# Kernel tuning notes

Measured on AMD Instinct MI355X. Metric: run time of the kernel, lower is better.

The kernel has to match this reference:

```python
import jax
import jax.numpy as jnp
import numpy as np

TOKENS, D_IN, D_OUT = 8192, 4096, 4096
QMAX = 127.0


def setup_inputs() -> dict:
    key = jax.random.key(0)
    k_x, k_w, k_s, k_o, k_b = jax.random.split(key, 5)
    x = jax.random.normal(k_x, (TOKENS, D_IN), dtype=jnp.float32)
    # int8-valued weight stored as int32 for portability (values in [-127, 127])
    weight = jax.random.randint(k_w, (D_OUT, D_IN), -127, 128, dtype=jnp.int32)
    # realistic small per-channel dequant scales
    weight_scale = (jax.random.uniform(k_s, (D_OUT,), dtype=jnp.float32) + 0.5) * 0.01
    # module stores -weight_offset; keep small integer-ish zero points
    weight_offset = jnp.round(jax.random.normal(k_o, (D_OUT,), dtype=jnp.float32) * 4.0)
    bias = jax.random.normal(k_b, (D_OUT,), dtype=jnp.float32) * 0.1
    return {"x": x, "weight": weight, "weight_scale": weight_scale,
            "weight_offset": weight_offset, "bias": bias}


def reference(x, weight, weight_scale, weight_offset, bias):
    # --- dynamic per-token symmetric activation quantization ---
    act_scale = jnp.max(jnp.abs(x), axis=-1, keepdims=True) / QMAX   # [T, 1]
    x_q = jnp.clip(jnp.round(x / act_scale), -QMAX, QMAX)            # int-valued fp32 [T, D_in]

    # --- int8 GEMM with per-channel zero-point correction ---
    # stored weight_offset = -zero_point, so dequant weight = scale * (w_q + weight_offset)
    acc = x_q @ weight.astype(jnp.float32).T                          # [T, D_out]
    zp_corr = jnp.sum(x_q, axis=-1, keepdims=True) * weight_offset[None, :]
    acc = acc + zp_corr

    # --- dequant + bias epilogue ---
    y = acc * act_scale * weight_scale[None, :] + bias[None, :]
    return y
```

## Files before the change

### kernel.cpp

```cpp
#include <hip/hip_runtime.h>
#include <cstdint>
#include <cstddef>

#define TOKENS 8192
#define DIN    4096
#define DOUT   4096

typedef int int4v  __attribute__((ext_vector_type(4)));
typedef int int16v __attribute__((ext_vector_type(16)));

__global__ __launch_bounds__(256) void quant_rows(const float* __restrict__ x,
                                                  int* __restrict__ xq,
                                                  float* __restrict__ ascale,
                                                  int* __restrict__ rsum) {
  const int row = blockIdx.x;
  const int t = threadIdx.x;
  const float4* xr = (const float4*)(x + (size_t)row * DIN);
  float4 v[4];
#pragma unroll
  for (int i = 0; i < 4; ++i) v[i] = xr[i * 256 + t];

  float m = 0.f;
#pragma unroll
  for (int i = 0; i < 4; ++i) {
    m = fmaxf(m, fabsf(v[i].x)); m = fmaxf(m, fabsf(v[i].y));
    m = fmaxf(m, fabsf(v[i].z)); m = fmaxf(m, fabsf(v[i].w));
  }
#pragma unroll
  for (int off = 32; off; off >>= 1) m = fmaxf(m, __shfl_xor(m, off));

  __shared__ float wmax[4];
  __shared__ int   wsum[4];
  const int lane = t & 63, wid = t >> 6;
  if (lane == 0) wmax[wid] = m;
  __syncthreads();
  m = fmaxf(fmaxf(wmax[0], wmax[1]), fmaxf(wmax[2], wmax[3]));

  const float s = m * (1.0f / 127.0f);
  const float sdiv = (m > 0.f) ? s : 1.0f;

  int ssum = 0;
#pragma unroll
  for (int i = 0; i < 4; ++i) {
    float q;
    q = fminf(fmaxf(rintf(v[i].x / sdiv), -127.f), 127.f); const int b0 = (int)q;
    q = fminf(fmaxf(rintf(v[i].y / sdiv), -127.f), 127.f); const int b1 = (int)q;
    q = fminf(fmaxf(rintf(v[i].z / sdiv), -127.f), 127.f); const int b2 = (int)q;
    q = fminf(fmaxf(rintf(v[i].w / sdiv), -127.f), 127.f); const int b3 = (int)q;
    ssum += b0 + b1 + b2 + b3;
    xq[(size_t)row * 1024 + i * 256 + t] =
        (b0 & 255) | ((b1 & 255) << 8) | ((b2 & 255) << 16) | ((b3 & 255) << 24);
  }
#pragma unroll
  for (int off = 32; off; off >>= 1) ssum += __shfl_xor(ssum, off);
  if (lane == 0) wsum[wid] = ssum;
  __syncthreads();
  if (t == 0) {
    rsum[row]   = wsum[0] + wsum[1] + wsum[2] + wsum[3];
    ascale[row] = s;
  }
}

__global__ __launch_bounds__(256) void wconv(const int* __restrict__ w,
                                             int* __restrict__ w8) {
  const int idx = blockIdx.x * 256 + threadIdx.x;
  const int4 v = ((const int4*)w)[idx];
  w8[idx] = (v.x & 255) | ((v.y & 255) << 8) | ((v.z & 255) << 16) | ((v.w & 255) << 24);
}

__device__ __forceinline__ void gload_lds16(const char* g, char* l) {
  __builtin_amdgcn_global_load_lds(
      (const __attribute__((address_space(1))) void*)g,
      (__attribute__((address_space(3))) void*)l, 16, 0, 0);
}

#define MFMA8(AV, BV)                                                         \
  __builtin_amdgcn_s_setprio(1);                                              \
  _Pragma("unroll")                                                           \
  for (int mi = 0; mi < 4; ++mi)                                              \
    _Pragma("unroll")                                                         \
    for (int ni = 0; ni < 2; ++ni)                                            \
      acc[mi][ni] = __builtin_amdgcn_mfma_i32_32x32x32_i8(                    \
          AV[mi], BV[ni], acc[mi][ni], 0, 0, 0);                              \
  __builtin_amdgcn_s_setprio(0);

#define TILE_BODY(T_, STAGE_, VMN_, NEXT_)                                    \
  do {                                                                        \
    const char* Lb = lds + ((T_) & 3) * 32768;                                \
    char* Wb = lds + (((T_) + 3) & 3) * 32768;                                \
    if (STAGE_) {                                                             \
      const size_t ko = (size_t)((T_) + 3) * 64;                              \
      gload_lds16(gA0 + ko, Wb + ldst);                                       \
      gload_lds16(gA1 + ko, Wb + 8192 + ldst);                                \
      gload_lds16(gB0 + ko, Wb + 16384 + ldst);                               \
      gload_lds16(gB1 + ko, Wb + 24576 + ldst);                               \
    }                                                                         \
    _Pragma("unroll")                                                         \
    for (int mi = 0; mi < 4; ++mi)                                            \
      aB[mi] = *(const int4v*)(Lb + aoff1 + mi * 2048);                       \
    _Pragma("unroll")                                                         \
    for (int ni = 0; ni < 2; ++ni)                                            \
      bB[ni] = *(const int4v*)(Lb + boff1 + ni * 2048);                       \
    MFMA8(aA, bA)                                                             \
    if (NEXT_) {                                                              \
      const char* Ln = lds + (((T_) + 1) & 3) * 32768;                        \
      _Pragma("unroll")                                                       \
      for (int mi = 0; mi < 4; ++mi)                                          \
        aA[mi] = *(const int4v*)(Ln + aoff0 + mi * 2048);                     \
      _Pragma("unroll")                                                       \
      for (int ni = 0; ni < 2; ++ni)                                          \
        bA[ni] = *(const int4v*)(Ln + boff0 + ni * 2048);                     \
    }                                                                         \
    MFMA8(aB, bB)                                                             \
    if ((VMN_) >= 0) {                                                        \
      if ((VMN_) == 4)      asm volatile("s_waitcnt vmcnt(4)" ::: "memory");  \
      else if ((VMN_) == 0) asm volatile("s_waitcnt vmcnt(0)" ::: "memory");  \
      __builtin_amdgcn_s_barrier();                                           \
    }                                                                         \
  } while (0)

__global__ __launch_bounds__(512, 2) void gemm_i8(
    const char* __restrict__ xq, const char* __restrict__ w8,
    const float* __restrict__ ascale, const int* __restrict__ rsum,
    const float* __restrict__ wscale, const float* __restrict__ woff,
    const float* __restrict__ bias, float* __restrict__ y) {

  __shared__ __align__(16) char lds[131072];

  const int bid = blockIdx.x;
  const int tm = bid >> 4;
  const int tn = bid & 15;
  const int t = threadIdx.x;
  const int lane = t & 63, wid = t >> 6;
  const int wmI = wid >> 2;
  const int wnI = wid & 3;

  const int S = (t * 16) ^ (((t >> 3) & 3) << 4) ^ (((t >> 6) & 1) << 6);
  const int srow = S >> 6;
  const int scol = S & 63;

  const char* gA0 = xq + (size_t)(tm * 256 + srow) * DIN + scol;
  const char* gA1 = gA0 + (size_t)128 * DIN;
  const char* gB0 = w8 + (size_t)(tn * 256 + srow) * DIN + scol;
  const char* gB1 = gB0 + (size_t)128 * DIN;
  const int ldst = t * 16;

  const int mask  = (((lane >> 1) & 3) << 4) ^ (((lane >> 4) & 1) << 6);
  const int arow  = (lane & 31) * 64 + (lane >> 5) * 16;
  const int aoff0 = wmI * 8192 + ((arow +  0) ^ mask);
  const int aoff1 = wmI * 8192 + ((arow + 32) ^ mask);
  const int brow  = (wnI & 1) * 4096 + arow;
  const int boff0 = (2 + (wnI >> 1)) * 8192 + ((brow +  0) ^ mask);
  const int boff1 = (2 + (wnI >> 1)) * 8192 + ((brow + 32) ^ mask);

  int16v acc[4][2];
#pragma unroll
  for (int mi = 0; mi < 4; ++mi)
#pragma unroll
    for (int ni = 0; ni < 2; ++ni)
#pragma unroll
      for (int rg = 0; rg < 16; ++rg) acc[mi][ni][rg] = 0;

  int4v aA[4], bA[2], aB[4], bB[2];

#pragma unroll
  for (int p = 0; p < 3; ++p) {
    char* Wb = lds + p * 32768;
    gload_lds16(gA0 + p * 64, Wb + ldst);
    gload_lds16(gA1 + p * 64, Wb + 8192 + ldst);
    gload_lds16(gB0 + p * 64, Wb + 16384 + ldst);
    gload_lds16(gB1 + p * 64, Wb + 24576 + ldst);
  }
  asm volatile("s_waitcnt vmcnt(4)" ::: "memory");
  __builtin_amdgcn_s_barrier();
#pragma unroll
  for (int mi = 0; mi < 4; ++mi) aA[mi] = *(const int4v*)(lds + aoff0 + mi * 2048);
#pragma unroll
  for (int ni = 0; ni < 2; ++ni) bA[ni] = *(const int4v*)(lds + boff0 + ni * 2048);

  for (int T = 0; T < 61; ++T) TILE_BODY(T, 1, 4, 1);
  TILE_BODY(61, 0, 0, 1);
  TILE_BODY(62, 0, -1, 1);
  TILE_BODY(63, 0, -1, 0);

  const int rb0 = tm * 256 + wmI * 128 + 4 * (lane >> 5);
  const int cb0 = tn * 256 + wnI * 64 + (lane & 31);
  const float ws0 = wscale[cb0],      ws1 = wscale[cb0 + 32];
  const float wo0 = woff[cb0],        wo1 = woff[cb0 + 32];
  const float bi0 = bias[cb0],        bi1 = bias[cb0 + 32];
#pragma unroll
  for (int mi = 0; mi < 4; ++mi) {
#pragma unroll
    for (int rg = 0; rg < 16; ++rg) {
      const int r = rb0 + mi * 32 + (rg & 3) + 8 * (rg >> 2);
      const float as_ = ascale[r];
      const float rs_ = (float)rsum[r];
      y[(size_t)r * DOUT + cb0]      = ((float)acc[mi][0][rg] + rs_ * wo0) * (as_ * ws0) + bi0;
      y[(size_t)r * DOUT + cb0 + 32] = ((float)acc[mi][1][rg] + rs_ * wo1) * (as_ * ws1) + bi1;
    }
  }
}

extern "C" void kernel_launch(void* const* d_in, const int* in_sizes, int n_in,
                              void* d_out, int out_size, void* d_ws, size_t ws_size,
                              hipStream_t stream) {
  const float* x      = (const float*)d_in[0];
  const int*   w      = (const int*)  d_in[1];
  const float* wscale = (const float*)d_in[2];
  const float* woff   = (const float*)d_in[3];
  const float* bias   = (const float*)d_in[4];
  float* y = (float*)d_out;

  char* ws = (char*)d_ws;
  char*  xq     = ws;
  char*  w8     = ws + (size_t)TOKENS * DIN;
  float* ascale = (float*)(w8 + (size_t)DOUT * DIN);
  int*   rsum   = (int*)(ascale + TOKENS);

  hipLaunchKernelGGL(quant_rows, dim3(TOKENS), dim3(256), 0, stream,
                     x, (int*)xq, ascale, rsum);
  hipLaunchKernelGGL(wconv, dim3((DOUT * DIN / 4) / 256), dim3(256), 0, stream,
                     w, (int*)w8);
  hipLaunchKernelGGL(gemm_i8, dim3((TOKENS / 256) * (DOUT / 256)), dim3(512), 0, stream,
                     xq, w8, ascale, rsum, wscale, woff, bias, y);
}
```

Before: 201.6 us.

## Load B operand directly from global into registers, stage only A via LDS

The weight (B) tile is no longer staged through LDS. Each wave now loads its own B fragments straight from global memory into registers, double-buffered one k-step ahead, while A keeps the LDS pipeline with half the LDS footprint. This removes the LDS traffic and bank pressure for B and frees LDS capacity. In exchange, B rows are reloaded from global/L2 by every wave that shares them instead of being shared through LDS. The vmcnt wait counts are adjusted to match the new number of in-flight loads.

```diff
diff --git a/kernel.cpp b/kernel.cpp
--- a/kernel.cpp
+++ b/kernel.cpp
@@ -68,55 +68,52 @@
   w8[idx] = (v.x & 255) | ((v.y & 255) << 8) | ((v.z & 255) << 16) | ((v.w & 255) << 24);
 }
 
-__device__ __forceinline__ void gload_lds16(const char* g, char* l) {
-  __builtin_amdgcn_global_load_lds(
-      (const __attribute__((address_space(1))) void*)g,
-      (__attribute__((address_space(3))) void*)l, 16, 0, 0);
-}
-
-#define MFMA8(AV, BV)                                                         \
-  __builtin_amdgcn_s_setprio(1);                                              \
-  _Pragma("unroll")                                                           \
-  for (int mi = 0; mi < 4; ++mi)                                              \
-    _Pragma("unroll")                                                         \
-    for (int ni = 0; ni < 2; ++ni)                                            \
-      acc[mi][ni] = __builtin_amdgcn_mfma_i32_32x32x32_i8(                    \
-          AV[mi], BV[ni], acc[mi][ni], 0, 0, 0);                              \
-  __builtin_amdgcn_s_setprio(0);
-
-#define TILE_BODY(T_, STAGE_, VMN_, NEXT_)                                    \
+#define GLOAD(G_, L_) __builtin_amdgcn_global_load_lds(                       \
+      (const __attribute__((address_space(1))) void*)(G_),                    \
+      (__attribute__((address_space(3))) void*)(L_), 16, 0, 0)
+
+#define TILE_BODY(T_, BC_, BN_, STG_, LDB_, LDA_, VMN_)                       \
   do {                                                                        \
-    const char* Lb = lds + ((T_) & 3) * 32768;                                \
-    char* Wb = lds + (((T_) + 3) & 3) * 32768;                                \
-    if (STAGE_) {                                                             \
+    const int rbO = ((T_) & 3) * 16384;                                       \
+    if (STG_) {                                                               \
+      char* Wb = lds + (((T_) + 3) & 3) * 16384;                              \
       const size_t ko = (size_t)((T_) + 3) * 64;                              \
-      gload_lds16(gA0 + ko, Wb + ldst);                                       \
-      gload_lds16(gA1 + ko, Wb + 8192 + ldst);                                \
-      gload_lds16(gB0 + ko, Wb + 16384 + ldst);                               \
-      gload_lds16(gB1 + ko, Wb + 24576 + ldst);                               \
+      GLOAD(gA0 + ko, Wb + ldst);                                             \
+      GLOAD(gA1 + ko, Wb + 8192 + ldst);                                      \
+    }                                                                         \
+    if (LDB_) {                                                               \
+      const size_t kb = (size_t)((T_) + 1) * 64;                              \
+      BN_[0] = *(const int4v*)(gB00 + kb);                                    \
+      BN_[1] = *(const int4v*)(gB10 + kb);                                    \
+      BN_[2] = *(const int4v*)(gB01 + kb);                                    \
+      BN_[3] = *(const int4v*)(gB11 + kb);                                    \
     }                                                                         \
     _Pragma("unroll")                                                         \
     for (int mi = 0; mi < 4; ++mi)                                            \
-      aB[mi] = *(const int4v*)(Lb + aoff1 + mi * 2048);                       \
+      aB[mi] = *(const int4v*)(lds + rbO + aoff1 + mi * 2048);                \
+    __builtin_amdgcn_s_setprio(1);                                            \
     _Pragma("unroll")                                                         \
-    for (int ni = 0; ni < 2; ++ni)                                            \
-      bB[ni] = *(const int4v*)(Lb + boff1 + ni * 2048);                       \
-    MFMA8(aA, bA)                                                             \
-    if (NEXT_) {                                                              \
-      const char* Ln = lds + (((T_) + 1) & 3) * 32768;                        \
+    for (int mi = 0; mi < 4; ++mi) {                                          \
+      acc[mi][0] = __builtin_amdgcn_mfma_i32_32x32x32_i8(aA[mi], BC_[0], acc[mi][0], 0, 0, 0); \
+      acc[mi][1] = __builtin_amdgcn_mfma_i32_32x32x32_i8(aA[mi], BC_[1], acc[mi][1], 0, 0, 0); \
+    }                                                                         \
+    __builtin_amdgcn_s_setprio(0);                                            \
+    if (LDA_) {                                                               \
+      const int rnO = (((T_) + 1) & 3) * 16384;                               \
       _Pragma("unroll")                                                       \
       for (int mi = 0; mi < 4; ++mi)                                          \
-        aA[mi] = *(const int4v*)(Ln + aoff0 + mi * 2048);                     \
-      _Pragma("unroll")                                                       \
-      for (int ni = 0; ni < 2; ++ni)                                          \
-        bA[ni] = *(const int4v*)(Ln + boff0 + ni * 2048);                     \
-    }                                                                         \
-    MFMA8(aB, bB)                                                             \
-    if ((VMN_) >= 0) {                                                        \
-      if ((VMN_) == 4)      asm volatile("s_waitcnt vmcnt(4)" ::: "memory");  \
-      else if ((VMN_) == 0) asm volatile("s_waitcnt vmcnt(0)" ::: "memory");  \
-      __builtin_amdgcn_s_barrier();                                           \
-    }                                                                         \
+        aA[mi] = *(const int4v*)(lds + rnO + aoff0 + mi * 2048);              \
+    }                                                                         \
+    __builtin_amdgcn_s_setprio(1);                                            \
+    _Pragma("unroll")                                                         \
+    for (int mi = 0; mi < 4; ++mi) {                                          \
+      acc[mi][0] = __builtin_amdgcn_mfma_i32_32x32x32_i8(aB[mi], BC_[2], acc[mi][0], 0, 0, 0); \
+      acc[mi][1] = __builtin_amdgcn_mfma_i32_32x32x32_i8(aB[mi], BC_[3], acc[mi][1], 0, 0, 0); \
+    }                                                                         \
+    __builtin_amdgcn_s_setprio(0);                                            \
+    if ((VMN_) == 6)      asm volatile("s_waitcnt vmcnt(6)" ::: "memory");    \
+    else if ((VMN_) == 4) asm volatile("s_waitcnt vmcnt(4)" ::: "memory");    \
+    if ((VMN_) >= 0) __builtin_amdgcn_s_barrier();                            \
   } while (0)
 
 __global__ __launch_bounds__(512, 2) void gemm_i8(
@@ -125,7 +122,7 @@
     const float* __restrict__ wscale, const float* __restrict__ woff,
     const float* __restrict__ bias, float* __restrict__ y) {
 
-  __shared__ __align__(16) char lds[131072];
+  __shared__ __align__(16) char lds[65536];
 
   const int bid = blockIdx.x;
   const int tm = bid >> 4;
@@ -141,17 +138,19 @@
 
   const char* gA0 = xq + (size_t)(tm * 256 + srow) * DIN + scol;
   const char* gA1 = gA0 + (size_t)128 * DIN;
-  const char* gB0 = w8 + (size_t)(tn * 256 + srow) * DIN + scol;
-  const char* gB1 = gB0 + (size_t)128 * DIN;
   const int ldst = t * 16;
 
   const int mask  = (((lane >> 1) & 3) << 4) ^ (((lane >> 4) & 1) << 6);
   const int arow  = (lane & 31) * 64 + (lane >> 5) * 16;
   const int aoff0 = wmI * 8192 + ((arow +  0) ^ mask);
   const int aoff1 = wmI * 8192 + ((arow + 32) ^ mask);
-  const int brow  = (wnI & 1) * 4096 + arow;
-  const int boff0 = (2 + (wnI >> 1)) * 8192 + ((brow +  0) ^ mask);
-  const int boff1 = (2 + (wnI >> 1)) * 8192 + ((brow + 32) ^ mask);
+
+  const char* gBL = w8 + (size_t)(tn * 256 + wnI * 64 + (lane & 31)) * DIN
+                       + (lane >> 5) * 16;
+  const char* gB00 = gBL;
+  const char* gB10 = gBL + 32 * DIN;
+  const char* gB01 = gBL + 32;
+  const char* gB11 = gBL + 32 * DIN + 32;
 
   int16v acc[4][2];
 #pragma unroll
@@ -161,27 +160,32 @@
 #pragma unroll
       for (int rg = 0; rg < 16; ++rg) acc[mi][ni][rg] = 0;
 
-  int4v aA[4], bA[2], aB[4], bB[2];
-
+  int4v aA[4], aB[4], bC[4], bN[4];
+
+  bC[0] = *(const int4v*)gB00;
+  bC[1] = *(const int4v*)gB10;
+  bC[2] = *(const int4v*)gB01;
+  bC[3] = *(const int4v*)gB11;
 #pragma unroll
   for (int p = 0; p < 3; ++p) {
-    char* Wb = lds + p * 32768;
-    gload_lds16(gA0 + p * 64, Wb + ldst);
-    gload_lds16(gA1 + p * 64, Wb + 8192 + ldst);
-    gload_lds16(gB0 + p * 64, Wb + 16384 + ldst);
-    gload_lds16(gB1 + p * 64, Wb + 24576 + ldst);
-  }
-  asm volatile("s_waitcnt vmcnt(4)" ::: "memory");
+    char* Wb = lds + p * 16384;
+    GLOAD(gA0 + p * 64, Wb + ldst);
+    GLOAD(gA1 + p * 64, Wb + 8192 + ldst);
+  }
+  asm volatile("s_waitcnt vmcnt(2)" ::: "memory");
   __builtin_amdgcn_s_barrier();
 #pragma unroll
-  for (int mi = 0; mi < 4; ++mi) aA[mi] = *(const int4v*)(lds + aoff0 + mi * 2048);
-#pragma unroll
-  for (int ni = 0; ni < 2; ++ni) bA[ni] = *(const int4v*)(lds + boff0 + ni * 2048);
-
-  for (int T = 0; T < 61; ++T) TILE_BODY(T, 1, 4, 1);
-  TILE_BODY(61, 0, 0, 1);
-  TILE_BODY(62, 0, -1, 1);
-  TILE_BODY(63, 0, -1, 0);
+  for (int mi = 0; mi < 4; ++mi)
+    aA[mi] = *(const int4v*)(lds + aoff0 + mi * 2048);
+
+  for (int T = 0; T < 60; T += 2) {
+    TILE_BODY(T,     bC, bN, 1, 1, 1, 6);
+    TILE_BODY(T + 1, bN, bC, 1, 1, 1, 6);
+  }
+  TILE_BODY(60, bC, bN, 1, 1, 1, 6);
+  TILE_BODY(61, bN, bC, 0, 1, 1, 4);
+  TILE_BODY(62, bC, bN, 0, 1, 1, -1);
+  TILE_BODY(63, bN, bC, 0, 0, 0, -1);
 
   const int rb0 = tm * 256 + wmI * 128 + 4 * (lane >> 5);
   const int cb0 = tn * 256 + wnI * 64 + (lane & 31);
```

Measured after the change: 243.9 us. +21.0%, slower.

## Process two K-tiles per barrier in int8 GEMM main loop

Applied to the files above, without the earlier changes.

Restructures the LDS pipeline of the int8 MFMA GEMM so each barrier step consumes two 64-wide K tiles instead of one. At the start of each step it issues global-to-LDS loads for the next two tiles, then waits for all outstanding loads and barriers once per pair. The prologue now prefetches four stages. This halves the number of workgroup barriers and waitcnts, but the loads for a pair now have only about one step to land before the full vmcnt(0) wait, which may expose more memory latency.

```diff
diff --git a/kernel.cpp b/kernel.cpp
--- a/kernel.cpp
+++ b/kernel.cpp
@@ -68,54 +68,60 @@
   w8[idx] = (v.x & 255) | ((v.y & 255) << 8) | ((v.z & 255) << 16) | ((v.w & 255) << 24);
 }
 
-__device__ __forceinline__ void gload_lds16(const char* g, char* l) {
-  __builtin_amdgcn_global_load_lds(
-      (const __attribute__((address_space(1))) void*)g,
-      (__attribute__((address_space(3))) void*)l, 16, 0, 0);
-}
-
-#define MFMA8(AV, BV)                                                         \
+#define GLOAD(G_, L_) __builtin_amdgcn_global_load_lds(                       \
+      (const __attribute__((address_space(1))) void*)(G_),                    \
+      (__attribute__((address_space(3))) void*)(L_), 16, 0, 0)
+
+#define RD(AV_, BV_, L_, AO_, BO_)                                            \
+    _Pragma("unroll")                                                         \
+    for (int mi = 0; mi < 4; ++mi)                                            \
+      AV_[mi] = *(const int4v*)((L_) + (AO_) + mi * 2048);                    \
+    _Pragma("unroll")                                                         \
+    for (int ni = 0; ni < 2; ++ni)                                            \
+      BV_[ni] = *(const int4v*)((L_) + (BO_) + ni * 2048);
+
+#define MFMA8(AV_, BV_)                                                       \
   __builtin_amdgcn_s_setprio(1);                                              \
   _Pragma("unroll")                                                           \
-  for (int mi = 0; mi < 4; ++mi)                                              \
-    _Pragma("unroll")                                                         \
-    for (int ni = 0; ni < 2; ++ni)                                            \
-      acc[mi][ni] = __builtin_amdgcn_mfma_i32_32x32x32_i8(                    \
-          AV[mi], BV[ni], acc[mi][ni], 0, 0, 0);                              \
+  for (int mi = 0; mi < 4; ++mi) {                                            \
+    acc[mi][0] = __builtin_amdgcn_mfma_i32_32x32x32_i8(AV_[mi], BV_[0], acc[mi][0], 0, 0, 0); \
+    acc[mi][1] = __builtin_amdgcn_mfma_i32_32x32x32_i8(AV_[mi], BV_[1], acc[mi][1], 0, 0, 0); \
+  }                                                                           \
   __builtin_amdgcn_s_setprio(0);
 
-#define TILE_BODY(T_, STAGE_, VMN_, NEXT_)                                    \
+#define SUPER(S_, STG_, BAR_)                                                 \
   do {                                                                        \
-    const char* Lb = lds + ((T_) & 3) * 32768;                                \
-    char* Wb = lds + (((T_) + 3) & 3) * 32768;                                \
-    if (STAGE_) {                                                             \
-      const size_t ko = (size_t)((T_) + 3) * 64;                              \
-      gload_lds16(gA0 + ko, Wb + ldst);                                       \
-      gload_lds16(gA1 + ko, Wb + 8192 + ldst);                                \
-      gload_lds16(gB0 + ko, Wb + 16384 + ldst);                               \
-      gload_lds16(gB1 + ko, Wb + 24576 + ldst);                               \
+    if (STG_) {                                                               \
+      char* W2 = lds + (((S_) + 2) & 3) * 32768;                              \
+      char* W3 = lds + (((S_) + 3) & 3) * 32768;                              \
+      const size_t k2 = (size_t)((S_) + 2) * 64;                              \
+      const size_t k3 = (size_t)((S_) + 3) * 64;                              \
+      GLOAD(gA0 + k2, W2 + ldst);                                             \
+      GLOAD(gA1 + k2, W2 + 8192 + ldst);                                      \
+      GLOAD(gB0 + k2, W2 + 16384 + ldst);                                     \
+      GLOAD(gB1 + k2, W2 + 24576 + ldst);                                     \
+      GLOAD(gA0 + k3, W3 + ldst);                                             \
+      GLOAD(gA1 + k3, W3 + 8192 + ldst);                                      \
+      GLOAD(gB0 + k3, W3 + 16384 + ldst);                                     \
+      GLOAD(gB1 + k3, W3 + 24576 + ldst);                                     \
     }                                                                         \
-    _Pragma("unroll")                                                         \
-    for (int mi = 0; mi < 4; ++mi)                                            \
-      aB[mi] = *(const int4v*)(Lb + aoff1 + mi * 2048);                       \
-    _Pragma("unroll")                                                         \
-    for (int ni = 0; ni < 2; ++ni)                                            \
-      bB[ni] = *(const int4v*)(Lb + boff1 + ni * 2048);                       \
-    MFMA8(aA, bA)                                                             \
-    if (NEXT_) {                                                              \
-      const char* Ln = lds + (((T_) + 1) & 3) * 32768;                        \
-      _Pragma("unroll")                                                       \
-      for (int mi = 0; mi < 4; ++mi)                                          \
-        aA[mi] = *(const int4v*)(Ln + aoff0 + mi * 2048);                     \
-      _Pragma("unroll")                                                       \
-      for (int ni = 0; ni < 2; ++ni)                                          \
-        bA[ni] = *(const int4v*)(Ln + boff0 + ni * 2048);                     \
+    {                                                                         \
+      const char* L0 = lds + ((S_) & 3) * 32768;                              \
+      const char* L1 = lds + (((S_) + 1) & 3) * 32768;                        \
+      RD(aB, bB, L0, aoff1, boff1)                               \
+      MFMA8(aA, bA)                                              \
+      RD(aA, bA, L1, aoff0, boff0)                               \
+      MFMA8(aB, bB)                                              \
+      RD(aB, bB, L1, aoff1, boff1)                               \
+      MFMA8(aA, bA)                                              \
+      MFMA8(aB, bB)                                              \
     }                                                                         \
-    MFMA8(aB, bB)                                                             \
-    if ((VMN_) >= 0) {                                                        \
-      if ((VMN_) == 4)      asm volatile("s_waitcnt vmcnt(4)" ::: "memory");  \
-      else if ((VMN_) == 0) asm volatile("s_waitcnt vmcnt(0)" ::: "memory");  \
+    if (BAR_) {                                                               \
+      asm volatile("s_waitcnt vmcnt(0)" ::: "memory");                        \
       __builtin_amdgcn_s_barrier();                                           \
+      __builtin_amdgcn_sched_barrier(0);                                      \
+      const char* L2 = lds + (((S_) + 2) & 3) * 32768;                        \
+      RD(aA, bA, L2, aoff0, boff0)                               \
     }                                                                         \
   } while (0)
 
@@ -135,9 +141,9 @@
   const int wmI = wid >> 2;
   const int wnI = wid & 3;
 
-  const int S = (t * 16) ^ (((t >> 3) & 3) << 4) ^ (((t >> 6) & 1) << 6);
-  const int srow = S >> 6;
-  const int scol = S & 63;
+  const int S_ = (t * 16) ^ (((t >> 3) & 3) << 4) ^ (((t >> 6) & 1) << 6);
+  const int srow = S_ >> 6;
+  const int scol = S_ & 63;
 
   const char* gA0 = xq + (size_t)(tm * 256 + srow) * DIN + scol;
   const char* gA1 = gA0 + (size_t)128 * DIN;
@@ -161,27 +167,25 @@
 #pragma unroll
       for (int rg = 0; rg < 16; ++rg) acc[mi][ni][rg] = 0;
 
-  int4v aA[4], bA[2], aB[4], bB[2];
-
-#pragma unroll
-  for (int p = 0; p < 3; ++p) {
+  int4v aA[4], aB[4], bA[2], bB[2];
+
+#pragma unroll
+  for (int p = 0; p < 4; ++p) {
     char* Wb = lds + p * 32768;
-    gload_lds16(gA0 + p * 64, Wb + ldst);
-    gload_lds16(gA1 + p * 64, Wb + 8192 + ldst);
-    gload_lds16(gB0 + p * 64, Wb + 16384 + ldst);
-    gload_lds16(gB1 + p * 64, Wb + 24576 + ldst);
-  }
-  asm volatile("s_waitcnt vmcnt(4)" ::: "memory");
+    GLOAD(gA0 + p * 64, Wb + ldst);
+    GLOAD(gA1 + p * 64, Wb + 8192 + ldst);
+    GLOAD(gB0 + p * 64, Wb + 16384 + ldst);
+    GLOAD(gB1 + p * 64, Wb + 24576 + ldst);
+  }
+  asm volatile("s_waitcnt vmcnt(8)" ::: "memory");
   __builtin_amdgcn_s_barrier();
-#pragma unroll
-  for (int mi = 0; mi < 4; ++mi) aA[mi] = *(const int4v*)(lds + aoff0 + mi * 2048);
-#pragma unroll
-  for (int ni = 0; ni < 2; ++ni) bA[ni] = *(const int4v*)(lds + boff0 + ni * 2048);
-
-  for (int T = 0; T < 61; ++T) TILE_BODY(T, 1, 4, 1);
-  TILE_BODY(61, 0, 0, 1);
-  TILE_BODY(62, 0, -1, 1);
-  TILE_BODY(63, 0, -1, 0);
+  __builtin_amdgcn_sched_barrier(0);
+  RD(aA, bA, lds, aoff0, boff0)
+
+  SUPER(0, 0, 1);
+  for (int S = 2; S <= 60; S += 2)
+    SUPER(S, 1, 1);
+  SUPER(62, 0, 0);
 
   const int rb0 = tm * 256 + wmI * 128 + 4 * (lane >> 5);
   const int cb0 = tn * 256 + wnI * 64 + (lane & 31);
```

Result: no change. 203.0 us (+0.7%).
